# Performance work log

Hardware: AMD Instinct MI355X
Metric: run time of the kernel (lower is better)

## Reference

```python
import jax, jax.numpy as jnp
import numpy as np

B, S, D, H = 2, 2048, 1024, 16
DH = D // H  # 64


def setup_inputs() -> dict:
    key = jax.random.key(0)
    ks = jax.random.split(key, 7)
    scale = 0.02
    return {
        "q": jax.random.normal(ks[0], (B, S, D), dtype=jnp.float32),
        "k": jax.random.normal(ks[1], (B, S, D), dtype=jnp.float32),
        "v": jax.random.normal(ks[2], (B, S, D), dtype=jnp.float32),
        "Wq": jax.random.normal(ks[3], (D, D), dtype=jnp.float32) * scale,
        "Wk": jax.random.normal(ks[4], (D, D), dtype=jnp.float32) * scale,
        "Wv": jax.random.normal(ks[5], (D, D), dtype=jnp.float32) * scale,
        "Wo": jax.random.normal(ks[6], (D, D), dtype=jnp.float32) * scale,
    }


def _split_heads(x):
    # [B, S, D] -> [B, H, S, DH]
    b, s, d = x.shape
    return x.reshape(b, s, H, DH).transpose(0, 2, 1, 3)


def reference(q, k, v, Wq, Wk, Wv, Wo):
    # Linear projections (torch Linear: x @ W.T, bias=False)
    qh = _split_heads(q @ Wq.T)  # [B, H, S, DH]
    kh = _split_heads(k @ Wk.T)
    vh = _split_heads(v @ Wv.T)
    # Scaled dot-product attention (manual, materializes scores as original)
    scores = jnp.einsum("bhqd,bhkd->bhqk", qh, kh) / jnp.sqrt(
        jnp.asarray(DH, dtype=qh.dtype)
    )  # [B, H, S, S]
    attn = jax.nn.softmax(scores, axis=-1)
    out = jnp.einsum("bhqk,bhkd->bhqd", attn, vh)  # [B, H, S, DH]
    # Concat heads: [B, H, S, DH] -> [B, S, D]
    out = out.transpose(0, 2, 1, 3).reshape(q.shape[0], q.shape[1], D)
    return out @ Wo.T
```

## Files before the change

kernel.cpp:

```cpp
#include <hip/hip_runtime.h>
#include <hip/hip_bf16.h>
#include <math.h>

namespace {
constexpr int Hn  = 16;
constexpr int DH  = 64;
constexpr int S   = 2048;
constexpr int D   = 1024;
constexpr int B   = 2;
constexpr int N   = B * S;
}

typedef __attribute__((ext_vector_type(8))) short bf16x8;
typedef __attribute__((ext_vector_type(4))) float f32x4;

#if defined(__has_builtin)
#if __has_builtin(__builtin_amdgcn_exp2f)
#define HAVE_EXP2_BUILTIN 1
#endif
#endif

static __device__ __forceinline__ float exp2_fast(float x) {
#ifdef HAVE_EXP2_BUILTIN
    return __builtin_amdgcn_exp2f(x);
#else
    float r;
    asm("v_exp_f32 %0, %1" : "=v"(r) : "v"(x));
    return r;
#endif
}

static __device__ __forceinline__ ushort bf16rd(float x) {
    unsigned u = __builtin_bit_cast(unsigned, x);
    return (ushort)((u + 0x8000u) >> 16);
}
static __device__ __forceinline__ float bfu2f(ushort h) {
    unsigned u = (unsigned)h << 16;
    return __builtin_bit_cast(float, u);
}
static __device__ __forceinline__ void split1(float a, ushort& h, ushort& l) {
    h = bf16rd(a);
    l = bf16rd(a - bfu2f(h));
}

static __device__ __forceinline__ void gload16(const ushort* g, ushort* l) {
    __builtin_amdgcn_global_load_lds((const unsigned int*)g, (unsigned int*)l, 16, 0, 0);
}

__global__ __launch_bounds__(256) void split_all(
    const float4* __restrict__ q, const float4* __restrict__ k, const float4* __restrict__ v,
    const float4* __restrict__ wq, const float4* __restrict__ wk,
    const float4* __restrict__ wv, const float4* __restrict__ wo,
    ushort4* __restrict__ qh, ushort4* __restrict__ kh, ushort4* __restrict__ vh,
    ushort4* __restrict__ wqh, ushort4* __restrict__ wkh, ushort4* __restrict__ wvh,
    ushort4* __restrict__ woh, ushort4* __restrict__ wol,
    int n4a, int n4w) {
    const int total = 3 * n4a + 4 * n4w;
    const int stride = gridDim.x * 256;
    for (int i = blockIdx.x * 256 + threadIdx.x; i < total; i += stride) {
        if (i < 3 * n4a) {
            const int which = i / n4a;
            const int j = i - which * n4a;
            const float4 val = (which == 0 ? q : which == 1 ? k : v)[j];
            ushort4* ph = which == 0 ? qh : which == 1 ? kh : vh;
            ph[j] = make_ushort4(bf16rd(val.x), bf16rd(val.y), bf16rd(val.z), bf16rd(val.w));
        } else {
            const int t = i - 3 * n4a;
            const int which = t / n4w;
            const int j = t - which * n4w;
            const float4 val = (which == 0 ? wq : which == 1 ? wk : which == 2 ? wv : wo)[j];
            if (which == 3) {
                ushort4 hh, ll;
                split1(val.x, hh.x, ll.x);
                split1(val.y, hh.y, ll.y);
                split1(val.z, hh.z, ll.z);
                split1(val.w, hh.w, ll.w);
                woh[j] = hh;
                wol[j] = ll;
            } else {
                ushort4* ph = which == 0 ? wqh : which == 1 ? wkh : wvh;
                ph[j] = make_ushort4(bf16rd(val.x), bf16rd(val.y), bf16rd(val.z), bf16rd(val.w));
            }
        }
    }
}

__global__ __launch_bounds__(256) void gemm_qkv(
    const ushort* __restrict__ qbf, const ushort* __restrict__ kbf,
    const ushort* __restrict__ vbf,
    const ushort* __restrict__ Wqh, const ushort* __restrict__ Wkh,
    const ushort* __restrict__ Wvh,
    ushort* __restrict__ Qbh, ushort* __restrict__ Kbh,
    ushort* __restrict__ Vtb, float qscale) {
    constexpr int BK = 32;
    constexpr int K = D;
    __shared__ __align__(16) ushort sA[128 * BK];
    __shared__ __align__(16) ushort sB[128 * BK];

    const int tid = threadIdx.x;
    const int which = blockIdx.y >> 3;
    const int m0 = blockIdx.x * 128;
    const int n0 = (blockIdx.y & 7) * 128;

    const ushort* A = which == 0 ? qbf : which == 1 ? kbf : vbf;
    const ushort* W = which == 0 ? Wqh : which == 1 ? Wkh : Wvh;

    const int l  = tid & 63;
    const int w  = tid >> 6;
    const int wm = w >> 1, wn = w & 1;
    const int lm = l & 15, g = l >> 4;

    const int srow = l >> 2;
    const int schunk = (l & 3) ^ ((l >> 3) & 3);
    const ushort* gA0 = A + (size_t)(m0 + w * 32 + srow) * K + schunk * 8;
    const ushort* gA1 = gA0 + (size_t)16 * K;
    const ushort* gB0 = W + (size_t)(n0 + w * 32 + srow) * K + schunk * 8;
    const ushort* gB1 = gB0 + (size_t)16 * K;
    ushort* lA0 = &sA[(w * 32) * BK];
    ushort* lA1 = &sA[(w * 32 + 16) * BK];
    ushort* lB0 = &sB[(w * 32) * BK];
    ushort* lB1 = &sB[(w * 32 + 16) * BK];

    const f32x4 fzero = {0.f, 0.f, 0.f, 0.f};
    f32x4 acc[4][4];
#pragma unroll
    for (int mi = 0; mi < 4; ++mi)
#pragma unroll
        for (int ni = 0; ni < 4; ++ni) acc[mi][ni] = fzero;

    const int sswz = (lm >> 1) & 3;

    for (int s = 0; s < K / BK; ++s) {
        const int k0 = s * BK;
        if (s) __syncthreads();
        gload16(gA0 + k0, lA0);
        gload16(gA1 + k0, lA1);
        gload16(gB0 + k0, lB0);
        gload16(gB1 + k0, lB1);
        __syncthreads();

        bf16x8 ah[4], bh[4];
#pragma unroll
        for (int mi = 0; mi < 4; ++mi)
            ah[mi] = *(const bf16x8*)&sA[(wm * 64 + mi * 16 + lm) * BK + (g ^ sswz) * 8];
#pragma unroll
        for (int ni = 0; ni < 4; ++ni)
            bh[ni] = *(const bf16x8*)&sB[(wn * 64 + ni * 16 + lm) * BK + (g ^ sswz) * 8];
        __builtin_amdgcn_s_setprio(1);
#pragma unroll
        for (int mi = 0; mi < 4; ++mi)
#pragma unroll
            for (int ni = 0; ni < 4; ++ni)
                acc[mi][ni] = __builtin_amdgcn_mfma_f32_16x16x32_bf16(
                    ah[mi], bh[ni], acc[mi][ni], 0, 0, 0);
        __builtin_amdgcn_s_setprio(0);
    }

#pragma unroll
    for (int mi = 0; mi < 4; ++mi)
#pragma unroll
        for (int ni = 0; ni < 4; ++ni) {
            const int col = n0 + wn * 64 + ni * 16 + lm;
            const int rbase = m0 + wm * 64 + mi * 16 + g * 4;
            const int hh = col >> 6, dh = col & (DH - 1);
            if (which == 0) {
#pragma unroll
                for (int r = 0; r < 4; ++r) {
                    const int row = rbase + r;
                    const int bb = row >> 11, ss = row & (S - 1);
                    const size_t idx = (((size_t)(bb * Hn + hh)) * S + ss) * DH + dh;
                    Qbh[idx] = bf16rd(acc[mi][ni][r] * qscale);
                }
            } else if (which == 1) {
#pragma unroll
                for (int r = 0; r < 4; ++r) {
                    const int row = rbase + r;
                    const int bb = row >> 11, ss = row & (S - 1);
                    const size_t idx = (((size_t)(bb * Hn + hh)) * S + ss) * DH + dh;
                    Kbh[idx] = bf16rd(acc[mi][ni][r]);
                }
            } else {
                const int bb = rbase >> 11, ss = rbase & (S - 1);
                ushort4 pk;
                pk.x = bf16rd(acc[mi][ni][0]);
                pk.y = bf16rd(acc[mi][ni][1]);
                pk.z = bf16rd(acc[mi][ni][2]);
                pk.w = bf16rd(acc[mi][ni][3]);
                const size_t idx = (((size_t)(bb * Hn + hh)) * DH + dh) * S + ss;
                *(ushort4*)&Vtb[idx] = pk;
            }
        }
}

__global__ __launch_bounds__(256) void gemm_out(const ushort* __restrict__ Ah,
                                                const ushort* __restrict__ Al,
                                                const ushort* __restrict__ Wh,
                                                const ushort* __restrict__ Wl,
                                                float* __restrict__ C) {
    constexpr int BK = 32;
    constexpr int LDT = 40;
    constexpr int K = D, O = D;
    __shared__ __align__(16) ushort sAh[2][128 * LDT];
    __shared__ __align__(16) ushort sAl[2][128 * LDT];
    __shared__ __align__(16) ushort sBh[2][64 * LDT];
    __shared__ __align__(16) ushort sBl[2][64 * LDT];

    const int tid = threadIdx.x;
    const int m0 = blockIdx.x * 128;
    const int n0 = blockIdx.y * 64;

    const int l   = tid & 63;
    const int wid = tid >> 6;
    const int wm  = wid >> 1;
    const int wn  = wid & 1;
    const int lm  = l & 15;
    const int g   = l >> 4;
    const int lk  = g * 8;

    const int arow0 = tid >> 2;
    const int aslot = (tid & 3) * 8;
    const ushort* gAh0 = Ah + (size_t)(m0 + arow0) * K + aslot;
    const ushort* gAh1 = gAh0 + (size_t)64 * K;
    const ushort* gAl0 = Al + (size_t)(m0 + arow0) * K + aslot;
    const ushort* gAl1 = gAl0 + (size_t)64 * K;
    const ushort* gBh  = Wh + (size_t)(n0 + arow0) * K + aslot;
    const ushort* gBl  = Wl + (size_t)(n0 + arow0) * K + aslot;

    const f32x4 fzero = {0.f, 0.f, 0.f, 0.f};
    f32x4 acc[4][2];
#pragma unroll
    for (int mi = 0; mi < 4; ++mi)
#pragma unroll
        for (int ni = 0; ni < 2; ++ni) acc[mi][ni] = fzero;

    uint4 rA0 = *(const uint4*)gAh0, rA1 = *(const uint4*)gAh1;
    uint4 rA2 = *(const uint4*)gAl0, rA3 = *(const uint4*)gAl1;
    uint4 rB0 = *(const uint4*)gBh,  rB1 = *(const uint4*)gBl;

    *(uint4*)&sAh[0][arow0 * LDT + aslot]        = rA0;
    *(uint4*)&sAh[0][(arow0 + 64) * LDT + aslot] = rA1;
    *(uint4*)&sAl[0][arow0 * LDT + aslot]        = rA2;
    *(uint4*)&sAl[0][(arow0 + 64) * LDT + aslot] = rA3;
    *(uint4*)&sBh[0][arow0 * LDT + aslot]        = rB0;
    *(uint4*)&sBl[0][arow0 * LDT + aslot]        = rB1;
    rA0 = *(const uint4*)(gAh0 + BK); rA1 = *(const uint4*)(gAh1 + BK);
    rA2 = *(const uint4*)(gAl0 + BK); rA3 = *(const uint4*)(gAl1 + BK);
    rB0 = *(const uint4*)(gBh + BK);  rB1 = *(const uint4*)(gBl + BK);
    __syncthreads();

    constexpr int NS = K / BK;
    int cur = 0;
    for (int s = 0; s < NS; ++s) {
        bf16x8 ah[4], al[4], bh[2], bl[2];
#pragma unroll
        for (int mi = 0; mi < 4; ++mi) {
            const int row = wm * 64 + mi * 16 + lm;
            ah[mi] = *(const bf16x8*)&sAh[cur][row * LDT + lk];
            al[mi] = *(const bf16x8*)&sAl[cur][row * LDT + lk];
        }
#pragma unroll
        for (int ni = 0; ni < 2; ++ni) {
            const int rowb = wn * 32 + ni * 16 + lm;
            bh[ni] = *(const bf16x8*)&sBh[cur][rowb * LDT + lk];
            bl[ni] = *(const bf16x8*)&sBl[cur][rowb * LDT + lk];
        }
        __builtin_amdgcn_s_setprio(1);
#pragma unroll
        for (int mi = 0; mi < 4; ++mi)
#pragma unroll
            for (int ni = 0; ni < 2; ++ni) {
                acc[mi][ni] = __builtin_amdgcn_mfma_f32_16x16x32_bf16(
                    al[mi], bh[ni], acc[mi][ni], 0, 0, 0);
                acc[mi][ni] = __builtin_amdgcn_mfma_f32_16x16x32_bf16(
                    ah[mi], bl[ni], acc[mi][ni], 0, 0, 0);
                acc[mi][ni] = __builtin_amdgcn_mfma_f32_16x16x32_bf16(
                    ah[mi], bh[ni], acc[mi][ni], 0, 0, 0);
            }
        __builtin_amdgcn_s_setprio(0);

        if (s < NS - 1) {
            const int nx = cur ^ 1;
            *(uint4*)&sAh[nx][arow0 * LDT + aslot]        = rA0;
            *(uint4*)&sAh[nx][(arow0 + 64) * LDT + aslot] = rA1;
            *(uint4*)&sAl[nx][arow0 * LDT + aslot]        = rA2;
            *(uint4*)&sAl[nx][(arow0 + 64) * LDT + aslot] = rA3;
            *(uint4*)&sBh[nx][arow0 * LDT + aslot]        = rB0;
            *(uint4*)&sBl[nx][arow0 * LDT + aslot]        = rB1;
            if (s < NS - 2) {
                const int kn = (s + 2) * BK;
                rA0 = *(const uint4*)(gAh0 + kn); rA1 = *(const uint4*)(gAh1 + kn);
                rA2 = *(const uint4*)(gAl0 + kn); rA3 = *(const uint4*)(gAl1 + kn);
                rB0 = *(const uint4*)(gBh + kn);  rB1 = *(const uint4*)(gBl + kn);
            }
            __syncthreads();
            cur = nx;
        }
    }

#pragma unroll
    for (int mi = 0; mi < 4; ++mi)
#pragma unroll
        for (int ni = 0; ni < 2; ++ni) {
            const int col = n0 + wn * 32 + ni * 16 + lm;
            const int rbase = m0 + wm * 64 + mi * 16 + g * 4;
#pragma unroll
            for (int r = 0; r < 4; ++r)
                C[(size_t)(rbase + r) * O + col] = acc[mi][ni][r];
        }
}

__global__ __launch_bounds__(256) void attn_mfma(const ushort* __restrict__ Qbh,
                                                 const ushort* __restrict__ Kbh,
                                                 const ushort* __restrict__ Vt,
                                                 ushort* __restrict__ AOh,
                                                 ushort* __restrict__ AOl) {
    constexpr int PLDT = 72;
    __shared__ __align__(16) ushort Ksh[2][64 * 64];
    __shared__ __align__(16) ushort Vts[2][64 * 64];
    __shared__ __align__(16) ushort Ps[128 * PLDT];

    const int tid = threadIdx.x;
    const int l = tid & 63, w = tid >> 6;
    const int g = l >> 4, l15 = l & 15;
    const int bh = blockIdx.x;
    const int q0 = blockIdx.y * 128;
    const size_t bhb = (size_t)bh * S * DH;

    bf16x8 qh_[2][2];
#pragma unroll
    for (int qb = 0; qb < 2; ++qb)
#pragma unroll
        for (int kk = 0; kk < 2; ++kk) {
            const size_t idx = bhb + (size_t)(q0 + w * 32 + qb * 16 + l15) * DH + kk * 32 + g * 8;
            qh_[qb][kk] = *(const bf16x8*)(Qbh + idx);
        }

    const int srow = l >> 3;
    const int schunk = (l & 7) ^ ((l >> 3) & 7);
    const ushort* Vb = Vt + (size_t)bh * DH * S;
    const ushort* gK0 = Kbh + bhb + (size_t)(w * 16 + srow) * DH + schunk * 8;
    const ushort* gK1 = gK0 + (size_t)8 * DH;
    const ushort* gV0 = Vb + (size_t)(w * 16 + srow) * S + schunk * 8;
    const ushort* gV1 = gV0 + (size_t)8 * S;

    const f32x4 fzero = {0.f, 0.f, 0.f, 0.f};
    f32x4 o_acc[2][4];
    f32x4 l_acc[2];
#pragma unroll
    for (int qb = 0; qb < 2; ++qb) {
        l_acc[qb] = fzero;
#pragma unroll
        for (int f = 0; f < 4; ++f) o_acc[qb][f] = fzero;
    }

    bf16x8 ones;
#pragma unroll
    for (int i = 0; i < 8; ++i) ones[i] = (short)0x3F80;

    auto stage = [&](int buf, int kt) {
        const size_t ko = (size_t)kt * 64 * DH;
        const size_t vo = (size_t)kt * 64;
        gload16(gK0 + ko, &Ksh[buf][(w * 16) * 64]);
        gload16(gK1 + ko, &Ksh[buf][(w * 16 + 8) * 64]);
        gload16(gV0 + vo, &Vts[buf][(w * 16) * 64]);
        gload16(gV1 + vo, &Vts[buf][(w * 16 + 8) * 64]);
    };

    stage(0, 0);
    __syncthreads();

    constexpr int NT = S / 64;
    int cur = 0;
    const int rsw = l15 & 7;
    for (int kt = 0; kt < NT; ++kt) {
        if (kt < NT - 1) stage(cur ^ 1, kt + 1);

        f32x4 sc[2][4];
#pragma unroll
        for (int qb = 0; qb < 2; ++qb)
#pragma unroll
            for (int f = 0; f < 4; ++f) sc[qb][f] = fzero;
#pragma unroll
        for (int kk = 0; kk < 2; ++kk) {
            bf16x8 kh[4];
#pragma unroll
            for (int f = 0; f < 4; ++f)
                kh[f] = *(const bf16x8*)&Ksh[cur][(f * 16 + l15) * 64 + ((kk * 4 + g) ^ rsw) * 8];
            __builtin_amdgcn_s_setprio(1);
#pragma unroll
            for (int f = 0; f < 4; ++f)
#pragma unroll
                for (int qb = 0; qb < 2; ++qb)
                    sc[qb][f] = __builtin_amdgcn_mfma_f32_16x16x32_bf16(
                        qh_[qb][kk], kh[f], sc[qb][f], 0, 0, 0);
            __builtin_amdgcn_s_setprio(0);
        }

#pragma unroll
        for (int qb = 0; qb < 2; ++qb)
#pragma unroll
            for (int f = 0; f < 4; ++f) {
#pragma unroll
                for (int r = 0; r < 4; ++r) {
                    const int prow = w * 32 + qb * 16 + g * 4 + r;
                    const int chunk = (f * 2 + (l15 >> 3)) ^ ((prow >> 2) & 7);
                    Ps[prow * PLDT + chunk * 8 + (l15 & 7)] =
                        bf16rd(exp2_fast(sc[qb][f][r]));
                }
            }

#pragma unroll
        for (int kk = 0; kk < 2; ++kk) {
            const int row0 = w * 32 + l15;
            const int row1 = row0 + 16;
            const int ck = kk * 4 + g;
            const bf16x8 pa0 = *(const bf16x8*)&Ps[row0 * PLDT + ((ck ^ ((row0 >> 2) & 7)) * 8)];
            const bf16x8 pa1 = *(const bf16x8*)&Ps[row1 * PLDT + ((ck ^ ((row1 >> 2) & 7)) * 8)];
            __builtin_amdgcn_s_setprio(1);
            l_acc[0] = __builtin_amdgcn_mfma_f32_16x16x32_bf16(pa0, ones, l_acc[0], 0, 0, 0);
            l_acc[1] = __builtin_amdgcn_mfma_f32_16x16x32_bf16(pa1, ones, l_acc[1], 0, 0, 0);
#pragma unroll
            for (int f = 0; f < 4; ++f) {
                const bf16x8 vt = *(const bf16x8*)&Vts[cur][(f * 16 + l15) * 64 + ((kk * 4 + g) ^ rsw) * 8];
                o_acc[0][f] = __builtin_amdgcn_mfma_f32_16x16x32_bf16(pa0, vt, o_acc[0][f], 0, 0, 0);
                o_acc[1][f] = __builtin_amdgcn_mfma_f32_16x16x32_bf16(pa1, vt, o_acc[1][f], 0, 0, 0);
            }
            __builtin_amdgcn_s_setprio(0);
        }

        if (kt < NT - 1) {
            __syncthreads();
            cur ^= 1;
        }
    }

    const int bb = bh >> 4, hh = bh & 15;
#pragma unroll
    for (int qb = 0; qb < 2; ++qb)
#pragma unroll
        for (int r = 0; r < 4; ++r) {
            const float inv = 1.f / l_acc[qb][r];
            const int row = q0 + w * 32 + qb * 16 + g * 4 + r;
#pragma unroll
            for (int f = 0; f < 4; ++f) {
                const float val = o_acc[qb][f][r] * inv;
                const size_t idx = ((size_t)(bb * S + row)) * D + hh * DH + f * 16 + l15;
                ushort hi, lo;
                split1(val, hi, lo);
                AOh[idx] = hi;
                AOl[idx] = lo;
            }
        }
}

extern "C" void kernel_launch(void* const* d_in, const int* in_sizes, int n_in,
                              void* d_out, int out_size, void* d_ws, size_t ws_size,
                              hipStream_t stream) {
    (void)in_sizes; (void)n_in; (void)out_size; (void)ws_size;
    const float* q  = (const float*)d_in[0];
    const float* k  = (const float*)d_in[1];
    const float* v  = (const float*)d_in[2];
    const float* Wq = (const float*)d_in[3];
    const float* Wk = (const float*)d_in[4];
    const float* Wv = (const float*)d_in[5];
    const float* Wo = (const float*)d_in[6];
    float* out = (float*)d_out;

    uint8_t* w8 = (uint8_t*)d_ws;
    constexpr size_t MB = 1u << 20;
    ushort* Wqh = (ushort*)(w8 + 0 * MB);
    ushort* Wkh = (ushort*)(w8 + 2 * MB);
    ushort* Wvh = (ushort*)(w8 + 4 * MB);
    ushort* Woh = (ushort*)(w8 + 6 * MB);
    ushort* Wol = (ushort*)(w8 + 8 * MB);
    ushort* qbf = (ushort*)(w8 + 16 * MB);
    ushort* kbf = (ushort*)(w8 + 24 * MB);
    ushort* vbf = (ushort*)(w8 + 32 * MB);
    ushort* Qbh = (ushort*)(w8 + 40 * MB);
    ushort* Kbh = (ushort*)(w8 + 48 * MB);
    ushort* Vtb = (ushort*)(w8 + 56 * MB);
    ushort* AOh = (ushort*)(w8 + 64 * MB);
    ushort* AOl = (ushort*)(w8 + 72 * MB);

    const int n4_act = (N * D) / 4;
    const int n4_w   = (D * D) / 4;
    const dim3 blk(256);

    split_all<<<2048, blk, 0, stream>>>(
        (const float4*)q, (const float4*)k, (const float4*)v,
        (const float4*)Wq, (const float4*)Wk, (const float4*)Wv, (const float4*)Wo,
        (ushort4*)qbf, (ushort4*)kbf, (ushort4*)vbf,
        (ushort4*)Wqh, (ushort4*)Wkh, (ushort4*)Wvh,
        (ushort4*)Woh, (ushort4*)Wol,
        n4_act, n4_w);

    const float qscale = 0.125f * 1.4426950408889634f;
    gemm_qkv<<<dim3(N / 128, 24), blk, 0, stream>>>(
        qbf, kbf, vbf, Wqh, Wkh, Wvh, Qbh, Kbh, Vtb, qscale);

    attn_mfma<<<dim3(B * Hn, S / 128), blk, 0, stream>>>(
        Qbh, Kbh, Vtb, AOh, AOl);

    gemm_out<<<dim3(N / 128, D / 64), blk, 0, stream>>>(AOh, AOl, Woh, Wol, out);
}
```

Before: 154.6 us.

## Double K-step in QKV GEMM and register-prefetch K/V tiles in attention

The QKV projection GEMM now uses a 64-wide K step with an 8-chunk XOR swizzle, which halves the number of barrier-separated iterations. The attention kernel drops the direct global-to-LDS async loads. Instead it prefetches K/V tiles two steps ahead into registers and writes them to padded (stride 72) LDS buffers after compute, hiding global latency behind the MFMA work. The cost is higher register pressure and extra LDS store instructions, and the padded layout replaces the swizzle for bank-conflict avoidance.

```diff
diff --git a/kernel.cpp b/kernel.cpp
--- a/kernel.cpp
+++ b/kernel.cpp
@@ -92,7 +92,7 @@
     const ushort* __restrict__ Wvh,
     ushort* __restrict__ Qbh, ushort* __restrict__ Kbh,
     ushort* __restrict__ Vtb, float qscale) {
-    constexpr int BK = 32;
+    constexpr int BK = 64;
     constexpr int K = D;
     __shared__ __align__(16) ushort sA[128 * BK];
     __shared__ __align__(16) ushort sB[128 * BK];
@@ -110,16 +110,12 @@
     const int wm = w >> 1, wn = w & 1;
     const int lm = l & 15, g = l >> 4;
 
-    const int srow = l >> 2;
-    const int schunk = (l & 3) ^ ((l >> 3) & 3);
-    const ushort* gA0 = A + (size_t)(m0 + w * 32 + srow) * K + schunk * 8;
-    const ushort* gA1 = gA0 + (size_t)16 * K;
-    const ushort* gB0 = W + (size_t)(n0 + w * 32 + srow) * K + schunk * 8;
-    const ushort* gB1 = gB0 + (size_t)16 * K;
-    ushort* lA0 = &sA[(w * 32) * BK];
-    ushort* lA1 = &sA[(w * 32 + 16) * BK];
-    ushort* lB0 = &sB[(w * 32) * BK];
-    ushort* lB1 = &sB[(w * 32 + 16) * BK];
+    const int srow = l >> 3;
+    const int schunk = (l & 7) ^ srow;
+    const ushort* gA = A + (size_t)(m0 + w * 32 + srow) * K + schunk * 8;
+    const ushort* gB = W + (size_t)(n0 + w * 32 + srow) * K + schunk * 8;
+    ushort* lA = &sA[(w * 32) * BK];
+    ushort* lB = &sB[(w * 32) * BK];
 
     const f32x4 fzero = {0.f, 0.f, 0.f, 0.f};
     f32x4 acc[4][4];
@@ -128,32 +124,36 @@
 #pragma unroll
         for (int ni = 0; ni < 4; ++ni) acc[mi][ni] = fzero;
 
-    const int sswz = (lm >> 1) & 3;
+    const int rsw = lm & 7;
 
     for (int s = 0; s < K / BK; ++s) {
         const int k0 = s * BK;
         if (s) __syncthreads();
-        gload16(gA0 + k0, lA0);
-        gload16(gA1 + k0, lA1);
-        gload16(gB0 + k0, lB0);
-        gload16(gB1 + k0, lB1);
+#pragma unroll
+        for (int j = 0; j < 4; ++j) {
+            gload16(gA + (size_t)(j * 8) * K + k0, lA + (j * 8) * BK);
+            gload16(gB + (size_t)(j * 8) * K + k0, lB + (j * 8) * BK);
+        }
         __syncthreads();
 
-        bf16x8 ah[4], bh[4];
-#pragma unroll
-        for (int mi = 0; mi < 4; ++mi)
-            ah[mi] = *(const bf16x8*)&sA[(wm * 64 + mi * 16 + lm) * BK + (g ^ sswz) * 8];
-#pragma unroll
-        for (int ni = 0; ni < 4; ++ni)
-            bh[ni] = *(const bf16x8*)&sB[(wn * 64 + ni * 16 + lm) * BK + (g ^ sswz) * 8];
-        __builtin_amdgcn_s_setprio(1);
-#pragma unroll
-        for (int mi = 0; mi < 4; ++mi)
+#pragma unroll
+        for (int kk = 0; kk < 2; ++kk) {
+            bf16x8 ah[4], bh[4];
+#pragma unroll
+            for (int mi = 0; mi < 4; ++mi)
+                ah[mi] = *(const bf16x8*)&sA[(wm * 64 + mi * 16 + lm) * BK + (((kk * 4 + g) ^ rsw) * 8)];
 #pragma unroll
             for (int ni = 0; ni < 4; ++ni)
-                acc[mi][ni] = __builtin_amdgcn_mfma_f32_16x16x32_bf16(
-                    ah[mi], bh[ni], acc[mi][ni], 0, 0, 0);
-        __builtin_amdgcn_s_setprio(0);
+                bh[ni] = *(const bf16x8*)&sB[(wn * 64 + ni * 16 + lm) * BK + (((kk * 4 + g) ^ rsw) * 8)];
+            __builtin_amdgcn_s_setprio(1);
+#pragma unroll
+            for (int mi = 0; mi < 4; ++mi)
+#pragma unroll
+                for (int ni = 0; ni < 4; ++ni)
+                    acc[mi][ni] = __builtin_amdgcn_mfma_f32_16x16x32_bf16(
+                        ah[mi], bh[ni], acc[mi][ni], 0, 0, 0);
+            __builtin_amdgcn_s_setprio(0);
+        }
     }
 
 #pragma unroll
@@ -314,10 +314,10 @@
                                                  const ushort* __restrict__ Vt,
                                                  ushort* __restrict__ AOh,
                                                  ushort* __restrict__ AOl) {
-    constexpr int PLDT = 72;
-    __shared__ __align__(16) ushort Ksh[2][64 * 64];
-    __shared__ __align__(16) ushort Vts[2][64 * 64];
-    __shared__ __align__(16) ushort Ps[128 * PLDT];
+    constexpr int LDT = 72;
+    __shared__ __align__(16) ushort Ksh[2][64 * LDT];
+    __shared__ __align__(16) ushort Vts[2][64 * LDT];
+    __shared__ __align__(16) ushort Ps[128 * LDT];
 
     const int tid = threadIdx.x;
     const int l = tid & 63, w = tid >> 6;
@@ -335,13 +335,13 @@
             qh_[qb][kk] = *(const bf16x8*)(Qbh + idx);
         }
 
-    const int srow = l >> 3;
-    const int schunk = (l & 7) ^ ((l >> 3) & 7);
-    const ushort* Vb = Vt + (size_t)bh * DH * S;
-    const ushort* gK0 = Kbh + bhb + (size_t)(w * 16 + srow) * DH + schunk * 8;
-    const ushort* gK1 = gK0 + (size_t)8 * DH;
-    const ushort* gV0 = Vb + (size_t)(w * 16 + srow) * S + schunk * 8;
-    const ushort* gV1 = gV0 + (size_t)8 * S;
+    const int r_st = tid >> 2;
+    const int c0 = (tid & 3) * 16;
+    const ushort* gKh = Kbh + bhb + (size_t)r_st * DH + c0;
+    const ushort* gVt = Vt + (size_t)bh * DH * S + (size_t)r_st * S + c0;
+
+    uint4 pk0 = *(const uint4*)gKh, pk1 = *(const uint4*)(gKh + 8);
+    uint4 pv0 = *(const uint4*)gVt, pv1 = *(const uint4*)(gVt + 8);
 
     const f32x4 fzero = {0.f, 0.f, 0.f, 0.f};
     f32x4 o_acc[2][4];
@@ -357,24 +357,17 @@
 #pragma unroll
     for (int i = 0; i < 8; ++i) ones[i] = (short)0x3F80;
 
-    auto stage = [&](int buf, int kt) {
-        const size_t ko = (size_t)kt * 64 * DH;
-        const size_t vo = (size_t)kt * 64;
-        gload16(gK0 + ko, &Ksh[buf][(w * 16) * 64]);
-        gload16(gK1 + ko, &Ksh[buf][(w * 16 + 8) * 64]);
-        gload16(gV0 + vo, &Vts[buf][(w * 16) * 64]);
-        gload16(gV1 + vo, &Vts[buf][(w * 16 + 8) * 64]);
-    };
-
-    stage(0, 0);
+    *(uint4*)&Ksh[0][r_st * LDT + c0]     = pk0;
+    *(uint4*)&Ksh[0][r_st * LDT + c0 + 8] = pk1;
+    *(uint4*)&Vts[0][r_st * LDT + c0]     = pv0;
+    *(uint4*)&Vts[0][r_st * LDT + c0 + 8] = pv1;
+    pk0 = *(const uint4*)(gKh + 64 * DH); pk1 = *(const uint4*)(gKh + 64 * DH + 8);
+    pv0 = *(const uint4*)(gVt + 64);      pv1 = *(const uint4*)(gVt + 64 + 8);
     __syncthreads();
 
     constexpr int NT = S / 64;
     int cur = 0;
-    const int rsw = l15 & 7;
     for (int kt = 0; kt < NT; ++kt) {
-        if (kt < NT - 1) stage(cur ^ 1, kt + 1);
-
         f32x4 sc[2][4];
 #pragma unroll
         for (int qb = 0; qb < 2; ++qb)
@@ -385,7 +378,7 @@
             bf16x8 kh[4];
 #pragma unroll
             for (int f = 0; f < 4; ++f)
-                kh[f] = *(const bf16x8*)&Ksh[cur][(f * 16 + l15) * 64 + ((kk * 4 + g) ^ rsw) * 8];
+                kh[f] = *(const bf16x8*)&Ksh[cur][(f * 16 + l15) * LDT + kk * 32 + g * 8];
             __builtin_amdgcn_s_setprio(1);
 #pragma unroll
             for (int f = 0; f < 4; ++f)
@@ -404,7 +397,7 @@
                 for (int r = 0; r < 4; ++r) {
                     const int prow = w * 32 + qb * 16 + g * 4 + r;
                     const int chunk = (f * 2 + (l15 >> 3)) ^ ((prow >> 2) & 7);
-                    Ps[prow * PLDT + chunk * 8 + (l15 & 7)] =
+                    Ps[prow * LDT + chunk * 8 + (l15 & 7)] =
                         bf16rd(exp2_fast(sc[qb][f][r]));
                 }
             }
@@ -414,14 +407,14 @@
             const int row0 = w * 32 + l15;
             const int row1 = row0 + 16;
             const int ck = kk * 4 + g;
-            const bf16x8 pa0 = *(const bf16x8*)&Ps[row0 * PLDT + ((ck ^ ((row0 >> 2) & 7)) * 8)];
-            const bf16x8 pa1 = *(const bf16x8*)&Ps[row1 * PLDT + ((ck ^ ((row1 >> 2) & 7)) * 8)];
+            const bf16x8 pa0 = *(const bf16x8*)&Ps[row0 * LDT + ((ck ^ ((row0 >> 2) & 7)) * 8)];
+            const bf16x8 pa1 = *(const bf16x8*)&Ps[row1 * LDT + ((ck ^ ((row1 >> 2) & 7)) * 8)];
             __builtin_amdgcn_s_setprio(1);
             l_acc[0] = __builtin_amdgcn_mfma_f32_16x16x32_bf16(pa0, ones, l_acc[0], 0, 0, 0);
             l_acc[1] = __builtin_amdgcn_mfma_f32_16x16x32_bf16(pa1, ones, l_acc[1], 0, 0, 0);
 #pragma unroll
             for (int f = 0; f < 4; ++f) {
-                const bf16x8 vt = *(const bf16x8*)&Vts[cur][(f * 16 + l15) * 64 + ((kk * 4 + g) ^ rsw) * 8];
+                const bf16x8 vt = *(const bf16x8*)&Vts[cur][(f * 16 + l15) * LDT + kk * 32 + g * 8];
                 o_acc[0][f] = __builtin_amdgcn_mfma_f32_16x16x32_bf16(pa0, vt, o_acc[0][f], 0, 0, 0);
                 o_acc[1][f] = __builtin_amdgcn_mfma_f32_16x16x32_bf16(pa1, vt, o_acc[1][f], 0, 0, 0);
             }
@@ -429,8 +422,19 @@
         }
 
         if (kt < NT - 1) {
+            const int nx = cur ^ 1;
+            *(uint4*)&Ksh[nx][r_st * LDT + c0]     = pk0;
+            *(uint4*)&Ksh[nx][r_st * LDT + c0 + 8] = pk1;
+            *(uint4*)&Vts[nx][r_st * LDT + c0]     = pv0;
+            *(uint4*)&Vts[nx][r_st * LDT + c0 + 8] = pv1;
+            if (kt < NT - 2) {
+                const int ok = (kt + 2) * 64 * DH;
+                const int ov = (kt + 2) * 64;
+                pk0 = *(const uint4*)(gKh + ok); pk1 = *(const uint4*)(gKh + ok + 8);
+                pv0 = *(const uint4*)(gVt + ov); pv1 = *(const uint4*)(gVt + ov + 8);
+            }
             __syncthreads();
-            cur ^= 1;
+            cur = nx;
         }
     }
 
```

After: 149.9 us. 1.03x faster.
